# Performance work log

Measured on AMD Instinct MI355X. Metric: run time of the kernel, lower is better.

The kernel has to match this reference:

```python
import jax, jax.numpy as jnp
import numpy as np

N = 50000   # nodes in both graphs
E = 800000  # edges per graph
IN = 128
OUT = 64
NEG_SLOPE = 0.2  # DGL GATConv default


def setup_inputs() -> dict:
    key = jax.random.key(0)
    ks = jax.random.split(key, 12)
    stdv = 1.0 / np.sqrt(OUT)
    return {
        'h': jax.random.normal(ks[0], (N, IN), dtype=jnp.float32),
        'src0': jax.random.randint(ks[1], (E,), 0, N, dtype=jnp.int32),
        'dst0': jax.random.randint(ks[2], (E,), 0, N, dtype=jnp.int32),
        'row2': jax.random.randint(ks[3], (E,), 0, N, dtype=jnp.int32),
        'col2': jax.random.randint(ks[4], (E,), 0, N, dtype=jnp.int32),
        'adj_val': jax.random.uniform(ks[5], (E,), dtype=jnp.float32),
        # GATConv params (1 head)
        'W_gat': jax.random.normal(ks[6], (IN, OUT), dtype=jnp.float32) * 0.1,
        'attn_l': jax.random.normal(ks[7], (OUT,), dtype=jnp.float32) * 0.1,
        'attn_r': jax.random.normal(ks[8], (OUT,), dtype=jnp.float32) * 0.1,
        'bias_gat': jnp.zeros((OUT,), dtype=jnp.float32),
        # GraphConvolution params
        'W_gc': jax.random.uniform(ks[9], (IN, OUT), minval=-stdv, maxval=stdv, dtype=jnp.float32),
        'bias_gc': jax.random.uniform(ks[10], (OUT,), minval=-stdv, maxval=stdv, dtype=jnp.float32),
    }


def reference(h, src0, dst0, row2, col2, adj_val, W_gat, attn_l, attn_r, bias_gat, W_gc, bias_gc):
    n = h.shape[0]
    # ---- branch 0: GATConv(1 head) + elu activation ----
    feat = h @ W_gat                        # [N, OUT]
    el = feat @ attn_l                      # [N]
    er = feat @ attn_r                      # [N]
    e = el[src0] + er[dst0]                 # [E]
    e = jnp.where(e > 0, e, NEG_SLOPE * e)  # leaky_relu
    # edge softmax over incoming edges of each dst (stable)
    m = jax.ops.segment_max(e, dst0, num_segments=n)
    ex = jnp.exp(e - m[dst0])
    s = jax.ops.segment_sum(ex, dst0, num_segments=n)
    alpha = ex / s[dst0]                    # [E]
    agg = jax.ops.segment_sum(alpha[:, None] * feat[src0], dst0, num_segments=n)
    z1 = jax.nn.elu(agg + bias_gat)         # [N, OUT]
    # ---- branch 1: GraphConvolution: elu(adj @ (h @ W) + b) ----
    support = h @ W_gc                      # [N, OUT]
    gc = jax.ops.segment_sum(adj_val[:, None] * support[col2], row2, num_segments=n)
    z2 = jax.nn.elu(gc + bias_gc)           # [N, OUT]
    # ---- semantic attention tail (forward is just split+concat) ----
    return jnp.concatenate((z1, z2), axis=1)  # [N, 2*OUT]
```

## Files before the change

kernel.cpp:

```cpp
#include <hip/hip_runtime.h>
#include <hip/hip_bf16.h>
#include <math.h>

#define IN_F 128
#define OUT_F 64
#define BKT_SH 7
#define BKT_MASK 127
#define CHUNK 4096
#define MAXTB 1600
#define IDX_BITS 25

typedef __attribute__((ext_vector_type(8))) short bf16x8;
typedef __attribute__((ext_vector_type(4))) float f32x4;

__device__ inline short f2bf(float x) {
    __hip_bfloat16 b = __float2bfloat16(x);
    return *reinterpret_cast<short*>(&b);
}
__device__ inline float bflo(unsigned u) { return __uint_as_float(u << 16); }
__device__ inline float bfhi(unsigned u) { return __uint_as_float(u & 0xffff0000u); }

__global__ __launch_bounds__(256) void k_fused(const float* __restrict__ h,
                                               const float* __restrict__ Wg,
                                               const float* __restrict__ Wc,
                                               const float* __restrict__ attn_l,
                                               const float* __restrict__ attn_r,
                                               __hip_bfloat16* __restrict__ feat,
                                               __hip_bfloat16* __restrict__ support,
                                               float* __restrict__ el,
                                               float* __restrict__ er, int n, int G1,
                                               const int* __restrict__ dst0,
                                               const int* __restrict__ row2,
                                               int* __restrict__ bcnt,
                                               int* __restrict__ chunkhist,
                                               int NB, int E_) {
    __shared__ short Wl[16][128][8];
    __shared__ int hist[MAXTB];

    if ((int)blockIdx.x >= G1) {
        int TB = 2 * NB;
        int t = threadIdx.x;
        int chunk = (int)blockIdx.x - G1;
        for (int i = t; i < TB; i += 256) hist[i] = 0;
        __syncthreads();
        int e0 = chunk * CHUNK;
        for (int i = t; i < CHUNK; i += 256) {
            int e = e0 + i;
            if (e < E_) {
                atomicAdd(&hist[dst0[e] >> BKT_SH], 1);
                atomicAdd(&hist[NB + (row2[e] >> BKT_SH)], 1);
            }
        }
        __syncthreads();
        int* hrow = chunkhist + (size_t)chunk * TB;
        for (int b = t; b < TB; b += 256) {
            int c = hist[b];
            hrow[b] = c;
            if (c) atomicAdd(&bcnt[b], c);
        }
        return;
    }

    for (int i = threadIdx.x; i < 128 * 32; i += 256) {
        int k = i >> 5;
        int c4 = (i & 31) << 2;
        float4 v4 = (c4 < 64) ? *(const float4*)(Wg + k * 64 + c4)
                              : *(const float4*)(Wc + k * 64 + (c4 - 64));
        short* dst = &Wl[k >> 3][c4][k & 7];
        dst[0]  = f2bf(v4.x);
        dst[8]  = f2bf(v4.y);
        dst[16] = f2bf(v4.z);
        dst[24] = f2bf(v4.w);
    }
    __syncthreads();

    int lane = threadIdx.x & 63;
    int wv = threadIdx.x >> 6;
    int li = lane & 15, lg = lane >> 4;
    int row0 = blockIdx.x * 64 + wv * 16;

    f32x4 acc[8];
#pragma unroll
    for (int ct = 0; ct < 8; ++ct) acc[ct] = (f32x4){0.f, 0.f, 0.f, 0.f};

    int ar = row0 + li;
    if (ar >= n) ar = n - 1;
    const float* hrow = h + (size_t)ar * IN_F + lg * 8;
#pragma unroll
    for (int q = 0; q < 4; ++q) {
        float4 a0 = *(const float4*)(hrow + q * 32);
        float4 a1 = *(const float4*)(hrow + q * 32 + 4);
        bf16x8 af;
        af[0] = f2bf(a0.x); af[1] = f2bf(a0.y); af[2] = f2bf(a0.z); af[3] = f2bf(a0.w);
        af[4] = f2bf(a1.x); af[5] = f2bf(a1.y); af[6] = f2bf(a1.z); af[7] = f2bf(a1.w);
        int kg = q * 4 + lg;
#pragma unroll
        for (int ct = 0; ct < 8; ++ct) {
            bf16x8 bfr = *(const bf16x8*)&Wl[kg][ct * 16 + li][0];
            acc[ct] = __builtin_amdgcn_mfma_f32_16x16x32_bf16(af, bfr, acc[ct], 0, 0, 0);
        }
    }

    float alv[4], arv[4];
#pragma unroll
    for (int ct = 0; ct < 4; ++ct) {
        alv[ct] = attn_l[ct * 16 + li];
        arv[ct] = attn_r[ct * 16 + li];
    }
#pragma unroll
    for (int r = 0; r < 4; ++r) {
        int row = row0 + lg * 4 + r;
        float pl = 0.f, pr = 0.f;
#pragma unroll
        for (int ct = 0; ct < 4; ++ct) {
            pl += acc[ct][r] * alv[ct];
            pr += acc[ct][r] * arv[ct];
        }
#pragma unroll
        for (int m = 8; m; m >>= 1) {
            pl += __shfl_xor(pl, m);
            pr += __shfl_xor(pr, m);
        }
        if (li == 0 && row < n) { el[row] = pl; er[row] = pr; }
    }

#pragma unroll
    for (int r = 0; r < 4; ++r) {
        int row = row0 + lg * 4 + r;
        if (row >= n) continue;
#pragma unroll
        for (int ct = 0; ct < 4; ++ct)
            feat[(size_t)row * OUT_F + ct * 16 + li] = __float2bfloat16(acc[ct][r]);
#pragma unroll
        for (int ct = 4; ct < 8; ++ct)
            support[(size_t)row * OUT_F + (ct - 4) * 16 + li] = __float2bfloat16(acc[ct][r]);
    }
}

__global__ __launch_bounds__(256) void k_bscan(const int* __restrict__ bcnt,
                                               int* __restrict__ boffs, int nb2,
                                               int grand, int* __restrict__ offs, int tot) {
    __shared__ int sh[256];
    int t = threadIdx.x;
    int base = t * 8;
    int v[8];
    int sum = 0;
#pragma unroll
    for (int i = 0; i < 8; ++i) {
        int idx = base + i;
        v[i] = (idx < nb2) ? bcnt[idx] : 0;
        sum += v[i];
    }
    sh[t] = sum;
    __syncthreads();
    for (int off = 1; off < 256; off <<= 1) {
        int x = (t >= off) ? sh[t - off] : 0;
        __syncthreads();
        sh[t] += x;
        __syncthreads();
    }
    int run = sh[t] - sum;
#pragma unroll
    for (int i = 0; i < 8; ++i) {
        int idx = base + i;
        if (idx < nb2) boffs[idx] = run;
        run += v[i];
    }
    if (t == 0) { boffs[nb2] = grand; offs[tot] = grand; }
}

__global__ __launch_bounds__(256) void k_part(const int* __restrict__ src0,
                                              const int* __restrict__ dst0,
                                              const int* __restrict__ row2,
                                              const int* __restrict__ boffs,
                                              const int* __restrict__ chunkhist,
                                              int* __restrict__ gfill,
                                              unsigned* __restrict__ tmp, int NB, int E_) {
    __shared__ int hist[MAXTB];
    __shared__ int rbase[MAXTB];
    int TB = 2 * NB;
    int t = threadIdx.x;
    const int* hrow = chunkhist + (size_t)blockIdx.x * TB;
    for (int b = t; b < TB; b += 256) {
        int c = hrow[b];
        int bb = 0;
        if (c) bb = boffs[b] + atomicAdd(&gfill[b], c);
        rbase[b] = bb;
        hist[b] = 0;
    }
    __syncthreads();
    int e0 = blockIdx.x * CHUNK;
    for (int i = t; i < CHUNK; i += 256) {
        int e = e0 + i;
        if (e < E_) {
            int d = dst0[e];
            int b = d >> BKT_SH;
            int p = atomicAdd(&hist[b], 1);
            tmp[(size_t)rbase[b] + p] =
                ((unsigned)(d & BKT_MASK) << IDX_BITS) | (unsigned)src0[e];
            int r = row2[e];
            int b2 = NB + (r >> BKT_SH);
            int p2 = atomicAdd(&hist[b2], 1);
            tmp[(size_t)rbase[b2] + p2] =
                ((unsigned)(r & BKT_MASK) << IDX_BITS) | (unsigned)e;
        }
    }
}

__global__ __launch_bounds__(256) void k_bbuild(const unsigned* __restrict__ tmp,
                                                const int* __restrict__ boffs,
                                                int* __restrict__ offs,
                                                int* __restrict__ bkt, int NB, int n) {
    __shared__ int hcnt[128], hoff[128], hfill[128], sh[128];
    int b = blockIdx.x;
    int t = threadIdx.x;
    int base = boffs[b];
    int cnt = boffs[b + 1] - base;
    int nodeBase = (b < NB ? b : b - NB) << BKT_SH;
    int offsBase = (b < NB ? 0 : n) + nodeBase;

    if (t < 128) hcnt[t] = 0;
    __syncthreads();
    for (int i = t; i < cnt; i += 256)
        atomicAdd(&hcnt[tmp[(size_t)base + i] >> IDX_BITS], 1);
    __syncthreads();
    if (t < 128) sh[t] = hcnt[t];
    __syncthreads();
    for (int off = 1; off < 128; off <<= 1) {
        int x = (t < 128 && t >= off) ? sh[t - off] : 0;
        __syncthreads();
        if (t < 128) sh[t] += x;
        __syncthreads();
    }
    if (t < 128) {
        hoff[t] = sh[t] - hcnt[t];
        hfill[t] = 0;
        if (nodeBase + t < n) offs[offsBase + t] = base + hoff[t];
    }
    __syncthreads();
    for (int i = t; i < cnt; i += 256) {
        unsigned v = tmp[(size_t)base + i];
        unsigned loc = v >> IDX_BITS;
        int p = atomicAdd(&hfill[loc], 1);
        bkt[(size_t)base + hoff[loc] + p] = (int)(v & ((1u << IDX_BITS) - 1u));
    }
}

__global__ __launch_bounds__(256) void k_agg(const int* __restrict__ bkt,
                                             const int* __restrict__ offs,
                                             const float* __restrict__ el,
                                             const float* __restrict__ er,
                                             const __hip_bfloat16* __restrict__ feat,
                                             const __hip_bfloat16* __restrict__ support,
                                             const int* __restrict__ col2,
                                             const float* __restrict__ adj_val,
                                             const float* __restrict__ bias_gat,
                                             const float* __restrict__ bias_gc,
                                             float* __restrict__ out, int n) {
    int wave = (int)(((long long)blockIdx.x * blockDim.x + threadIdx.x) >> 6);
    int lane = threadIdx.x & 63;
    int nh = (n + 1) >> 1;
    if (wave >= 2 * nh) return;
    int half = lane >> 5;
    int ll = lane & 31;
    int es2 = ll >> 4;
    int fg = ll & 15;
    int sbase = half << 5;

    bool isGat = wave < nh;
    int node = (isGat ? wave : wave - nh) * 2 + half;
    bool nodeValid = node < n;
    int wid = (isGat ? 0 : n) + (nodeValid ? node : 0);
    int start = offs[wid];
    int deg = nodeValid ? offs[wid + 1] - start : 0;

    float acc[4] = {0.f, 0.f, 0.f, 0.f};

    if (isGat) {
        float erd = nodeValid ? er[node] : 0.f;
        float sw = 0.f;
        const uint2* fp = (const uint2*)feat;
        for (int c0 = 0; c0 < deg; c0 += 32) {
            int cnt = min(32, deg - c0);
            bool valid = ll < cnt;
            int s = valid ? bkt[start + c0 + ll] : 0;
            float v = (valid ? el[s] : 0.f) + erd;
            v = v > 0.f ? v : 0.2f * v;
            float w = valid ? __expf(v) : 0.f;
            float t = w;
            t += __shfl_xor(t, 1);  t += __shfl_xor(t, 2);
            t += __shfl_xor(t, 4);  t += __shfl_xor(t, 8);
            t += __shfl_xor(t, 16);
            sw += t;
#pragma unroll 4
            for (int k = 0; k < cnt; k += 2) {
                int src = sbase + k + es2;
                float wk = __shfl(w, src);
                int sk = __shfl(s, src);
                uint2 pv = fp[(size_t)sk * 16 + fg];
                acc[0] += wk * bflo(pv.x); acc[1] += wk * bfhi(pv.x);
                acc[2] += wk * bflo(pv.y); acc[3] += wk * bfhi(pv.y);
            }
        }
#pragma unroll
        for (int j = 0; j < 4; ++j) acc[j] += __shfl_xor(acc[j], 16);
        if (es2 == 0 && nodeValid) {
            float inv = deg > 0 ? __builtin_amdgcn_rcpf(sw) : 0.f;
            float4 bb = *(const float4*)(bias_gat + fg * 4);
            float z0 = acc[0] * inv + bb.x;
            float z1 = acc[1] * inv + bb.y;
            float z2 = acc[2] * inv + bb.z;
            float z3 = acc[3] * inv + bb.w;
            z0 = z0 > 0.f ? z0 : __expf(z0) - 1.f;
            z1 = z1 > 0.f ? z1 : __expf(z1) - 1.f;
            z2 = z2 > 0.f ? z2 : __expf(z2) - 1.f;
            z3 = z3 > 0.f ? z3 : __expf(z3) - 1.f;
            *(float4*)(out + (size_t)node * 128 + fg * 4) = make_float4(z0, z1, z2, z3);
        }
    } else {
        const uint2* sp = (const uint2*)support;
        for (int c0 = 0; c0 < deg; c0 += 32) {
            int cnt = min(32, deg - c0);
            bool valid = ll < cnt;
            int eid = valid ? bkt[start + c0 + ll] : 0;
            float a = valid ? adj_val[eid] : 0.f;
            int c = valid ? col2[eid] : 0;
#pragma unroll 4
            for (int k = 0; k < cnt; k += 2) {
                int src = sbase + k + es2;
                float ak = __shfl(a, src);
                int ck = __shfl(c, src);
                uint2 pv = sp[(size_t)ck * 16 + fg];
                acc[0] += ak * bflo(pv.x); acc[1] += ak * bfhi(pv.x);
                acc[2] += ak * bflo(pv.y); acc[3] += ak * bfhi(pv.y);
            }
        }
#pragma unroll
        for (int j = 0; j < 4; ++j) acc[j] += __shfl_xor(acc[j], 16);
        if (es2 == 0 && nodeValid) {
            float4 bb = *(const float4*)(bias_gc + fg * 4);
            float z0 = acc[0] + bb.x;
            float z1 = acc[1] + bb.y;
            float z2 = acc[2] + bb.z;
            float z3 = acc[3] + bb.w;
            z0 = z0 > 0.f ? z0 : __expf(z0) - 1.f;
            z1 = z1 > 0.f ? z1 : __expf(z1) - 1.f;
            z2 = z2 > 0.f ? z2 : __expf(z2) - 1.f;
            z3 = z3 > 0.f ? z3 : __expf(z3) - 1.f;
            *(float4*)(out + (size_t)node * 128 + OUT_F + fg * 4) = make_float4(z0, z1, z2, z3);
        }
    }
}

extern "C" void kernel_launch(void* const* d_in, const int* in_sizes, int n_in,
                              void* d_out, int out_size, void* d_ws, size_t ws_size,
                              hipStream_t stream) {
    const float* h        = (const float*)d_in[0];
    const int*   src0     = (const int*)d_in[1];
    const int*   dst0     = (const int*)d_in[2];
    const int*   row2     = (const int*)d_in[3];
    const int*   col2     = (const int*)d_in[4];
    const float* adj_val  = (const float*)d_in[5];
    const float* Wg       = (const float*)d_in[6];
    const float* attn_l   = (const float*)d_in[7];
    const float* attn_r   = (const float*)d_in[8];
    const float* bias_gat = (const float*)d_in[9];
    const float* Wc       = (const float*)d_in[10];
    const float* bias_gc  = (const float*)d_in[11];

    int n  = in_sizes[0] / IN_F;
    int E_ = in_sizes[1];
    float* out = (float*)d_out;

    int NB = (n + BKT_MASK) >> BKT_SH;
    int TB = 2 * NB;
    if (TB > MAXTB) return;
    if (n >= (1 << IDX_BITS) || E_ >= (1 << IDX_BITS)) return;

    int nchunk = (E_ + CHUNK - 1) / CHUNK;

    char* p = (char*)d_ws;
    auto alloc = [&](size_t bytes, size_t align) -> void* {
        size_t a = ((size_t)p + align - 1) & ~(align - 1);
        p = (char*)(a + bytes);
        return (void*)a;
    };
    unsigned* tmp = (unsigned*)alloc(2 * (size_t)E_ * sizeof(unsigned), 256);
    int*   bkt   = (int*)  alloc(2 * (size_t)E_ * sizeof(int), 16);
    int*   offs  = (int*)  alloc((2 * (size_t)n + 1) * sizeof(int), 16);
    float* el    = (float*)alloc((size_t)n * sizeof(float), 16);
    float* er    = (float*)alloc((size_t)n * sizeof(float), 16);
    int*   bcnt  = (int*)  alloc(2 * (size_t)TB * sizeof(int), 16);
    int*   gfill = bcnt + TB;
    int*   boffs = (int*)  alloc(((size_t)TB + 1) * sizeof(int), 16);
    int*   chunkhist = (int*)alloc((size_t)nchunk * TB * sizeof(int), 16);
    __hip_bfloat16* feat    = (__hip_bfloat16*)alloc((size_t)n * OUT_F * sizeof(__hip_bfloat16), 256);
    __hip_bfloat16* support = (__hip_bfloat16*)alloc((size_t)n * OUT_F * sizeof(__hip_bfloat16), 256);
    size_t need = (size_t)(p - (char*)d_ws);
    if (ws_size < need) return;

    int G1 = (n + 63) / 64;

    hipMemsetAsync(bcnt, 0, 2 * (size_t)TB * sizeof(int), stream);
    k_fused<<<G1 + nchunk, 256, 0, stream>>>(h, Wg, Wc, attn_l, attn_r,
                                             feat, support, el, er, n, G1,
                                             dst0, row2, bcnt, chunkhist, NB, E_);
    k_bscan<<<1, 256, 0, stream>>>(bcnt, boffs, TB, 2 * E_, offs, 2 * n);
    k_part<<<nchunk, 256, 0, stream>>>(src0, dst0, row2, boffs, chunkhist,
                                       gfill, tmp, NB, E_);
    k_bbuild<<<TB, 256, 0, stream>>>(tmp, boffs, offs, bkt, NB, n);
    int nh = (n + 1) >> 1;
    long long aggthreads = 2LL * nh * 64;
    k_agg<<<(int)((aggthreads + 255) / 256), 256, 0, stream>>>(
        bkt, offs, el, er, feat, support, col2, adj_val, bias_gat, bias_gc, out, n);
}
```

Baseline: 133.0 us.

## Fuse bucket build and aggregation into one kernel with LDS edge payloads

Merges the per-bucket counting sort (k_bbuild) with the aggregation kernel (k_agg). Each block now sorts its 128-node bucket locally and stores (index, weight) pairs in LDS, falling back to a global buffer when a bucket exceeds CAP. The exp attention weights and col2/adj_val gathers are computed once per edge during the sort. This removes a kernel launch, the global bkt/offs round trip and per-wave redundant loads. In exchange there are fewer, larger blocks (TB ≈ 782) with heavy LDS use, which may lower occupancy and load balance compared with one wave per node pair.

```diff
diff --git a/kernel.cpp b/kernel.cpp
--- a/kernel.cpp
+++ b/kernel.cpp
@@ -9,6 +9,7 @@
 #define CHUNK 4096
 #define MAXTB 1600
 #define IDX_BITS 25
+#define CAP 3072
 
 typedef __attribute__((ext_vector_type(8))) short bf16x8;
 typedef __attribute__((ext_vector_type(4))) float f32x4;
@@ -139,7 +140,7 @@
 
 __global__ __launch_bounds__(256) void k_bscan(const int* __restrict__ bcnt,
                                                int* __restrict__ boffs, int nb2,
-                                               int grand, int* __restrict__ offs, int tot) {
+                                               int grand) {
     __shared__ int sh[256];
     int t = threadIdx.x;
     int base = t * 8;
@@ -166,7 +167,7 @@
         if (idx < nb2) boffs[idx] = run;
         run += v[i];
     }
-    if (t == 0) { boffs[nb2] = grand; offs[tot] = grand; }
+    if (t == 0) boffs[nb2] = grand;
 }
 
 __global__ __launch_bounds__(256) void k_part(const int* __restrict__ src0,
@@ -207,106 +208,106 @@
     }
 }
 
-__global__ __launch_bounds__(256) void k_bbuild(const unsigned* __restrict__ tmp,
-                                                const int* __restrict__ boffs,
-                                                int* __restrict__ offs,
-                                                int* __restrict__ bkt, int NB, int n) {
-    __shared__ int hcnt[128], hoff[128], hfill[128], sh[128];
+__global__ __launch_bounds__(256) void k_bagg(const unsigned* __restrict__ tmp,
+                                              const int* __restrict__ boffs,
+                                              const float* __restrict__ el,
+                                              const float* __restrict__ er,
+                                              const __hip_bfloat16* __restrict__ feat,
+                                              const __hip_bfloat16* __restrict__ support,
+                                              const int* __restrict__ col2,
+                                              const float* __restrict__ adj_val,
+                                              const float* __restrict__ bias_gat,
+                                              const float* __restrict__ bias_gc,
+                                              int2* __restrict__ ewg,
+                                              float* __restrict__ out, int NB, int n) {
+    __shared__ int2 ew_lds[CAP + 1];
+    __shared__ int hcnt[128], hoff[128], hfill[128], shs[128];
+    __shared__ float er_lds[128];
     int b = blockIdx.x;
     int t = threadIdx.x;
     int base = boffs[b];
     int cnt = boffs[b + 1] - base;
-    int nodeBase = (b < NB ? b : b - NB) << BKT_SH;
-    int offsBase = (b < NB ? 0 : n) + nodeBase;
-
-    if (t < 128) hcnt[t] = 0;
+    bool isGat = b < NB;
+    int nodeBase = (isGat ? b : b - NB) << BKT_SH;
+
+    if (t < 128) {
+        hcnt[t] = 0;
+        hfill[t] = 0;
+        if (isGat && nodeBase + t < n) er_lds[t] = er[nodeBase + t];
+    }
     __syncthreads();
     for (int i = t; i < cnt; i += 256)
         atomicAdd(&hcnt[tmp[(size_t)base + i] >> IDX_BITS], 1);
     __syncthreads();
-    if (t < 128) sh[t] = hcnt[t];
+    if (t < 128) shs[t] = hcnt[t];
     __syncthreads();
     for (int off = 1; off < 128; off <<= 1) {
-        int x = (t < 128 && t >= off) ? sh[t - off] : 0;
-        __syncthreads();
-        if (t < 128) sh[t] += x;
-        __syncthreads();
-    }
-    if (t < 128) {
-        hoff[t] = sh[t] - hcnt[t];
-        hfill[t] = 0;
-        if (nodeBase + t < n) offs[offsBase + t] = base + hoff[t];
-    }
-    __syncthreads();
+        int x = (t < 128 && t >= off) ? shs[t - off] : 0;
+        __syncthreads();
+        if (t < 128) shs[t] += x;
+        __syncthreads();
+    }
+    if (t < 128) hoff[t] = shs[t] - hcnt[t];
+    __syncthreads();
+
+    int2* ews = (cnt <= CAP) ? (int2*)ew_lds : (ewg + base);
     for (int i = t; i < cnt; i += 256) {
         unsigned v = tmp[(size_t)base + i];
         unsigned loc = v >> IDX_BITS;
-        int p = atomicAdd(&hfill[loc], 1);
-        bkt[(size_t)base + hoff[loc] + p] = (int)(v & ((1u << IDX_BITS) - 1u));
-    }
-}
-
-__global__ __launch_bounds__(256) void k_agg(const int* __restrict__ bkt,
-                                             const int* __restrict__ offs,
-                                             const float* __restrict__ el,
-                                             const float* __restrict__ er,
-                                             const __hip_bfloat16* __restrict__ feat,
-                                             const __hip_bfloat16* __restrict__ support,
-                                             const int* __restrict__ col2,
-                                             const float* __restrict__ adj_val,
-                                             const float* __restrict__ bias_gat,
-                                             const float* __restrict__ bias_gc,
-                                             float* __restrict__ out, int n) {
-    int wave = (int)(((long long)blockIdx.x * blockDim.x + threadIdx.x) >> 6);
-    int lane = threadIdx.x & 63;
-    int nh = (n + 1) >> 1;
-    if (wave >= 2 * nh) return;
-    int half = lane >> 5;
-    int ll = lane & 31;
+        int idx = (int)(v & ((1u << IDX_BITS) - 1u));
+        int pdst = hoff[loc] + atomicAdd(&hfill[loc], 1);
+        int2 payload;
+        if (isGat) {
+            float e = el[idx] + er_lds[loc];
+            e = e > 0.f ? e : 0.2f * e;
+            payload = make_int2(idx, __float_as_int(__expf(e)));
+        } else {
+            payload = make_int2(col2[idx], __float_as_int(adj_val[idx]));
+        }
+        ews[pdst] = payload;
+    }
+    __syncthreads();
+
+    int hw = t >> 5;
+    int ll = t & 31;
     int es2 = ll >> 4;
     int fg = ll & 15;
-    int sbase = half << 5;
-
-    bool isGat = wave < nh;
-    int node = (isGat ? wave : wave - nh) * 2 + half;
-    bool nodeValid = node < n;
-    int wid = (isGat ? 0 : n) + (nodeValid ? node : 0);
-    int start = offs[wid];
-    int deg = nodeValid ? offs[wid + 1] - start : 0;
-
-    float acc[4] = {0.f, 0.f, 0.f, 0.f};
-
-    if (isGat) {
-        float erd = nodeValid ? er[node] : 0.f;
+    const uint2* fbase = (const uint2*)(isGat ? feat : support);
+    const float* bias = isGat ? bias_gat : bias_gc;
+    float4 bb = *(const float4*)(bias + fg * 4);
+    int outoff = isGat ? 0 : OUT_F;
+
+    for (int loc = hw; loc < 128; loc += 8) {
+        int node = nodeBase + loc;
+        if (node >= n) break;
+        int start = hoff[loc], deg = hcnt[loc];
+        float acc[4] = {0.f, 0.f, 0.f, 0.f};
         float sw = 0.f;
-        const uint2* fp = (const uint2*)feat;
         for (int c0 = 0; c0 < deg; c0 += 32) {
-            int cnt = min(32, deg - c0);
-            bool valid = ll < cnt;
-            int s = valid ? bkt[start + c0 + ll] : 0;
-            float v = (valid ? el[s] : 0.f) + erd;
-            v = v > 0.f ? v : 0.2f * v;
-            float w = valid ? __expf(v) : 0.f;
-            float t = w;
-            t += __shfl_xor(t, 1);  t += __shfl_xor(t, 2);
-            t += __shfl_xor(t, 4);  t += __shfl_xor(t, 8);
-            t += __shfl_xor(t, 16);
-            sw += t;
+            int c = min(32, deg - c0);
+            if (isGat) {
+                float w = (ll < c) ? __int_as_float(ews[start + c0 + ll].y) : 0.f;
+                float ts = w;
+                ts += __shfl_xor(ts, 1);  ts += __shfl_xor(ts, 2);
+                ts += __shfl_xor(ts, 4);  ts += __shfl_xor(ts, 8);
+                ts += __shfl_xor(ts, 16);
+                sw += ts;
+            }
 #pragma unroll 4
-            for (int k = 0; k < cnt; k += 2) {
-                int src = sbase + k + es2;
-                float wk = __shfl(w, src);
-                int sk = __shfl(s, src);
-                uint2 pv = fp[(size_t)sk * 16 + fg];
+            for (int k = 0; k < c; k += 2) {
+                bool ok = (k + es2) < c;
+                int ei = ok ? (start + c0 + k + es2) : start;
+                int2 e = ews[ei];
+                float wk = ok ? __int_as_float(e.y) : 0.f;
+                uint2 pv = fbase[(size_t)e.x * 16 + fg];
                 acc[0] += wk * bflo(pv.x); acc[1] += wk * bfhi(pv.x);
                 acc[2] += wk * bflo(pv.y); acc[3] += wk * bfhi(pv.y);
             }
         }
 #pragma unroll
         for (int j = 0; j < 4; ++j) acc[j] += __shfl_xor(acc[j], 16);
-        if (es2 == 0 && nodeValid) {
-            float inv = deg > 0 ? __builtin_amdgcn_rcpf(sw) : 0.f;
-            float4 bb = *(const float4*)(bias_gat + fg * 4);
+        if (es2 == 0) {
+            float inv = isGat ? (deg > 0 ? __builtin_amdgcn_rcpf(sw) : 0.f) : 1.f;
             float z0 = acc[0] * inv + bb.x;
             float z1 = acc[1] * inv + bb.y;
             float z2 = acc[2] * inv + bb.z;
@@ -315,39 +316,8 @@
             z1 = z1 > 0.f ? z1 : __expf(z1) - 1.f;
             z2 = z2 > 0.f ? z2 : __expf(z2) - 1.f;
             z3 = z3 > 0.f ? z3 : __expf(z3) - 1.f;
-            *(float4*)(out + (size_t)node * 128 + fg * 4) = make_float4(z0, z1, z2, z3);
-        }
-    } else {
-        const uint2* sp = (const uint2*)support;
-        for (int c0 = 0; c0 < deg; c0 += 32) {
-            int cnt = min(32, deg - c0);
-            bool valid = ll < cnt;
-            int eid = valid ? bkt[start + c0 + ll] : 0;
-            float a = valid ? adj_val[eid] : 0.f;
-            int c = valid ? col2[eid] : 0;
-#pragma unroll 4
-            for (int k = 0; k < cnt; k += 2) {
-                int src = sbase + k + es2;
-                float ak = __shfl(a, src);
-                int ck = __shfl(c, src);
-                uint2 pv = sp[(size_t)ck * 16 + fg];
-                acc[0] += ak * bflo(pv.x); acc[1] += ak * bfhi(pv.x);
-                acc[2] += ak * bflo(pv.y); acc[3] += ak * bfhi(pv.y);
-            }
-        }
-#pragma unroll
-        for (int j = 0; j < 4; ++j) acc[j] += __shfl_xor(acc[j], 16);
-        if (es2 == 0 && nodeValid) {
-            float4 bb = *(const float4*)(bias_gc + fg * 4);
-            float z0 = acc[0] + bb.x;
-            float z1 = acc[1] + bb.y;
-            float z2 = acc[2] + bb.z;
-            float z3 = acc[3] + bb.w;
-            z0 = z0 > 0.f ? z0 : __expf(z0) - 1.f;
-            z1 = z1 > 0.f ? z1 : __expf(z1) - 1.f;
-            z2 = z2 > 0.f ? z2 : __expf(z2) - 1.f;
-            z3 = z3 > 0.f ? z3 : __expf(z3) - 1.f;
-            *(float4*)(out + (size_t)node * 128 + OUT_F + fg * 4) = make_float4(z0, z1, z2, z3);
+            *(float4*)(out + (size_t)node * 128 + outoff + fg * 4) =
+                make_float4(z0, z1, z2, z3);
         }
     }
 }
@@ -386,8 +356,7 @@
         return (void*)a;
     };
     unsigned* tmp = (unsigned*)alloc(2 * (size_t)E_ * sizeof(unsigned), 256);
-    int*   bkt   = (int*)  alloc(2 * (size_t)E_ * sizeof(int), 16);
-    int*   offs  = (int*)  alloc((2 * (size_t)n + 1) * sizeof(int), 16);
+    int2*  ewg   = (int2*) alloc((2 * (size_t)E_ + 1) * sizeof(int2), 256);
     float* el    = (float*)alloc((size_t)n * sizeof(float), 16);
     float* er    = (float*)alloc((size_t)n * sizeof(float), 16);
     int*   bcnt  = (int*)  alloc(2 * (size_t)TB * sizeof(int), 16);
@@ -405,12 +374,10 @@
     k_fused<<<G1 + nchunk, 256, 0, stream>>>(h, Wg, Wc, attn_l, attn_r,
                                              feat, support, el, er, n, G1,
                                              dst0, row2, bcnt, chunkhist, NB, E_);
-    k_bscan<<<1, 256, 0, stream>>>(bcnt, boffs, TB, 2 * E_, offs, 2 * n);
+    k_bscan<<<1, 256, 0, stream>>>(bcnt, boffs, TB, 2 * E_);
     k_part<<<nchunk, 256, 0, stream>>>(src0, dst0, row2, boffs, chunkhist,
                                        gfill, tmp, NB, E_);
-    k_bbuild<<<TB, 256, 0, stream>>>(tmp, boffs, offs, bkt, NB, n);
-    int nh = (n + 1) >> 1;
-    long long aggthreads = 2LL * nh * 64;
-    k_agg<<<(int)((aggthreads + 255) / 256), 256, 0, stream>>>(
-        bkt, offs, el, er, feat, support, col2, adj_val, bias_gat, bias_gc, out, n);
-}
+    k_bagg<<<TB, 256, 0, stream>>>(tmp, boffs, el, er, feat, support,
+                                   col2, adj_val, bias_gat, bias_gc,
+                                   ewg, out, NB, n);
+}
```

Result: slower. 152.0 us (+14.3%).
